# Performance work log

Hardware: AMD Instinct MI355X
Metric: run time of the kernel (lower is better)

The kernel has to match this reference:

```python
import jax, jax.numpy as jnp
import numpy as np

B, L_R, H = 8, 128, 512
CTX_LEN, STATE_NUM, ACT_NUM = 256, 32, 32
L_SRC = CTX_LEN + STATE_NUM + ACT_NUM
N_VOCAB = 32000
N_TOPIC = 4096


def setup_inputs() -> dict:
    key = jax.random.key(0)
    ks = jax.random.split(key, 9)
    return {
        "dec_out": jax.random.normal(ks[0], (B, L_R, H), jnp.float32),
        "src_hidden": jax.random.normal(ks[1], (B, L_SRC, H), jnp.float32),
        "W_gen": jax.random.normal(ks[2], (H, N_VOCAB), jnp.float32) * 0.02,
        "b_gen": jnp.zeros((N_VOCAB,), jnp.float32),
        "src_mask": jax.random.randint(ks[3], (B, 1, L_SRC), 0, 2, jnp.int32),
        "context": jax.random.randint(ks[4], (B, CTX_LEN), 0, N_VOCAB, jnp.int32),
        "tp": jax.random.randint(ks[5], (B, STATE_NUM), 0, N_TOPIC, jnp.int32),
        "action": jax.random.randint(ks[6], (B, ACT_NUM), 0, N_TOPIC, jnp.int32),
        "loc2glo": jax.random.randint(ks[7], (N_TOPIC,), 0, N_VOCAB, jnp.int32),
    }


def _scatter_vocab(prob, idx):
    # prob: [L_r, L_seg], idx: [L_seg] global-vocab ids -> [L_r, n_vocab]
    # duplicate indices accumulate, matching torch scatter_add / one-hot bmm
    return jnp.zeros((prob.shape[0], N_VOCAB), prob.dtype).at[:, idx].add(prob)


def reference(dec_out, src_hidden, W_gen, b_gen, src_mask, context, tp, action, loc2glo):
    # gen logits: [B, L_r, n_vocab]
    gen_logit = jnp.einsum("blh,hv->blv", dec_out, W_gen) + b_gen
    # copy logits over concatenated source: [B, L_r, L_src]
    copy_logit = jnp.einsum("blh,bsh->bls", dec_out, src_hidden)
    copy_logit = jnp.where(src_mask == 0, jnp.float32(-1e9), copy_logit)
    logits = jnp.concatenate([gen_logit, copy_logit], axis=-1)
    logits = logits * (H ** -0.5)  # op.scale_prj
    probs = jax.nn.softmax(logits, axis=-1)

    gen_prob = probs[:, :, :N_VOCAB]
    copy_ctx = probs[:, :, N_VOCAB:N_VOCAB + CTX_LEN]
    copy_tp = probs[:, :, N_VOCAB + CTX_LEN:N_VOCAB + CTX_LEN + STATE_NUM]
    copy_ar = probs[:, :, N_VOCAB + CTX_LEN + STATE_NUM:]

    scatter = jax.vmap(_scatter_vocab)
    ctx_prob = scatter(copy_ctx, context)                 # replaces one-hot bmm
    tp_prob = scatter(copy_tp, loc2glo[tp])               # scatter_add via loc2glo gather
    ar_prob = scatter(copy_ar, loc2glo[action])

    return gen_prob + ctx_prob + tp_prob + ar_prob
```

## Files before the change

kernel.cpp:

```cpp
#include <hip/hip_runtime.h>
#include <stdint.h>
#include <stddef.h>

#define NV    32000
#define HDIM  512
#define LSRC  320
#define MROWS 1024
#define SCALEF 0.044194173824159216f

typedef unsigned short u16;
typedef unsigned int   u32;
typedef __attribute__((ext_vector_type(8))) short short8;
typedef __attribute__((ext_vector_type(4))) float floatx4;

__device__ __forceinline__ u16 f2bf(float f) {
  u32 x = __float_as_uint(f);
  return (u16)((x + 0x7fffu + ((x >> 16) & 1u)) >> 16);
}

typedef __attribute__((address_space(1))) void gvoid;
typedef __attribute__((address_space(3))) void lvoid;
__device__ __forceinline__ void cp16(const u16* g, u16* l) {
  __builtin_amdgcn_global_load_lds((gvoid*)g, (lvoid*)l, 16, 0, 0);
}

__global__ __launch_bounds__(256) void k_convA(const float* __restrict__ dec,
                                               u16* __restrict__ Ab,
                                               float* __restrict__ rowSum) {
  if (blockIdx.x == 0) {
    ((float4*)rowSum)[threadIdx.x] = (float4){0.f, 0.f, 0.f, 0.f};
  }
  int t = blockIdx.x * 256 + threadIdx.x;
  int o = t * 8;
  int tile = o >> 12;
  int mt = tile >> 4, kt = tile & 15;
  int mi = (o & 4095) >> 5, ki = o & 31;
  const float* s = dec + (size_t)(mt * 128 + mi) * HDIM + kt * 32 + ki;
  float4 a = ((const float4*)s)[0];
  float4 b = ((const float4*)s)[1];
  union { u16 h[8]; uint4 v; } pk;
  pk.h[0] = f2bf(a.x); pk.h[1] = f2bf(a.y); pk.h[2] = f2bf(a.z); pk.h[3] = f2bf(a.w);
  pk.h[4] = f2bf(b.x); pk.h[5] = f2bf(b.y); pk.h[6] = f2bf(b.z); pk.h[7] = f2bf(b.w);
  *(uint4*)(Ab + o) = pk.v;
}

__global__ __launch_bounds__(256) void k_convW(const float* __restrict__ W,
                                               u16* __restrict__ Wb) {
  __shared__ u16 lds[128 * 36];
  int tileId = blockIdx.x;
  int nt = tileId >> 4, kt = tileId & 15;
  int t = threadIdx.x;
  const float* src = W + (size_t)kt * 32 * NV + (size_t)nt * 128;
#pragma unroll
  for (int i = 0; i < 4; ++i) {
    int f = t + 256 * i;
    int kin = f >> 5, n4 = f & 31;
    float4 v = *(const float4*)(src + (size_t)kin * NV + n4 * 4);
    int base = (n4 * 4) * 36 + kin;
    lds[base]       = f2bf(v.x);
    lds[base + 36]  = f2bf(v.y);
    lds[base + 72]  = f2bf(v.z);
    lds[base + 108] = f2bf(v.w);
  }
  __syncthreads();
  u16* dst = Wb + (size_t)tileId * 4096;
#pragma unroll
  for (int j = 0; j < 2; ++j) {
    int o = t * 8 + j * 2048;
    int ni = o >> 5, ki0 = o & 31;
    const u16* p = &lds[ni * 36 + ki0];
    uint2 x = *(const uint2*)p;
    uint2 y = *(const uint2*)(p + 4);
    uint4 v; v.x = x.x; v.y = x.y; v.z = y.x; v.w = y.y;
    *(uint4*)(dst + o) = v;
  }
}

__global__ __launch_bounds__(256) void k_convS(const float* __restrict__ srch,
                                               u16* __restrict__ Sb) {
  int t = blockIdx.x * 256 + threadIdx.x;
  int o = t * 8;
  int ki = o & 31;
  int ni = (o >> 5) & 127;
  int kt = (o >> 12) & 15;
  int r  = o >> 16;
  int tile = r % 3, b = r / 3;
  int s = tile * 128 + ni;
  uint4 v;
  if (s < LSRC) {
    const float* p = srch + ((size_t)b * LSRC + s) * HDIM + kt * 32 + ki;
    float4 a = ((const float4*)p)[0];
    float4 c = ((const float4*)p)[1];
    union { u16 h[8]; uint4 u; } pk;
    pk.h[0] = f2bf(a.x); pk.h[1] = f2bf(a.y); pk.h[2] = f2bf(a.z); pk.h[3] = f2bf(a.w);
    pk.h[4] = f2bf(c.x); pk.h[5] = f2bf(c.y); pk.h[6] = f2bf(c.z); pk.h[7] = f2bf(c.w);
    v = pk.u;
  } else {
    v = (uint4){0u, 0u, 0u, 0u};
  }
  *(uint4*)(Sb + o) = v;
}

__global__ __launch_bounds__(256) void k_gemm(const u16* __restrict__ Ab,
                                              const u16* __restrict__ Wb,
                                              const u16* __restrict__ Sb,
                                              const float* __restrict__ bgen,
                                              const int* __restrict__ mask,
                                              u16* __restrict__ wsE,
                                              float* __restrict__ wsCopy,
                                              float* __restrict__ rowSum) {
  __shared__ u16 As[3][4096];
  __shared__ u16 Bs[3][4096];
  int bid = blockIdx.x;
  int x = (bid >> 3) & 7;
  int y = ((bid >> 6) << 3) | (bid & 7);
  if (y >= 253) return;
  int t = threadIdx.x;
  int wid = t >> 6, lane = t & 63;
  int wm = wid >> 1, wn = wid & 1;
  int quad = lane >> 4, l16 = lane & 15;

  const u16* At = Ab + (size_t)x * (16 * 4096);
  const u16* Bt = (y < 250) ? (Wb + (size_t)y * (16 * 4096))
                            : (Sb + (size_t)(x * 3 + (y - 250)) * (16 * 4096));
  const u16* Ag0 = At + wid * 1024 + lane * 8;
  const u16* Bg0 = Bt + wid * 1024 + lane * 8;

  floatx4 acc[4][4];
#pragma unroll
  for (int i = 0; i < 4; ++i)
#pragma unroll
    for (int j = 0; j < 4; ++j) acc[i][j] = (floatx4){0.f, 0.f, 0.f, 0.f};

#pragma unroll
  for (int p = 0; p < 2; ++p) {
    const u16* ag = Ag0 + p * 4096;
    const u16* bg = Bg0 + p * 4096;
    cp16(ag,       &As[p][wid * 1024]);
    cp16(ag + 512, &As[p][wid * 1024 + 512]);
    cp16(bg,       &Bs[p][wid * 1024]);
    cp16(bg + 512, &Bs[p][wid * 1024 + 512]);
  }

#pragma unroll
  for (int kt = 0; kt < 16; ++kt) {
    const int cb = kt % 3;
    asm volatile("s_waitcnt lgkmcnt(0)" ::: "memory");
    if (kt < 15) asm volatile("s_waitcnt vmcnt(4)" ::: "memory");
    else         asm volatile("s_waitcnt vmcnt(0)" ::: "memory");
    __builtin_amdgcn_s_barrier();
    asm volatile("" ::: "memory");
    if (kt < 14) {
      const int sb = (kt + 2) % 3;
      const u16* ag = Ag0 + (kt + 2) * 4096;
      const u16* bg = Bg0 + (kt + 2) * 4096;
      cp16(ag,       &As[sb][wid * 1024]);
      cp16(ag + 512, &As[sb][wid * 1024 + 512]);
      cp16(bg,       &Bs[sb][wid * 1024]);
      cp16(bg + 512, &Bs[sb][wid * 1024 + 512]);
    }
    short8 aR[4], bR[4];
#pragma unroll
    for (int mt = 0; mt < 4; ++mt)
      aR[mt] = *(const short8*)&As[cb][(wm * 64 + mt * 16 + l16) * 32 + quad * 8];
#pragma unroll
    for (int nt = 0; nt < 4; ++nt)
      bR[nt] = *(const short8*)&Bs[cb][(wn * 64 + nt * 16 + l16) * 32 + quad * 8];
#pragma unroll
    for (int mt = 0; mt < 4; ++mt)
#pragma unroll
      for (int nt = 0; nt < 4; ++nt)
        acc[mt][nt] = __builtin_amdgcn_mfma_f32_16x16x32_bf16(aR[mt], bR[nt],
                                                              acc[mt][nt], 0, 0, 0);
  }

  int row0 = x * 128 + wm * 64;
  if (y < 250) {
    int col0 = y * 128 + wn * 64;
    float bg[4];
#pragma unroll
    for (int nt = 0; nt < 4; ++nt) bg[nt] = bgen[col0 + nt * 16 + l16];
#pragma unroll
    for (int mt = 0; mt < 4; ++mt) {
      float rs[4] = {0.f, 0.f, 0.f, 0.f};
#pragma unroll
      for (int nt = 0; nt < 4; ++nt) {
        int col = col0 + nt * 16 + l16;
#pragma unroll
        for (int r = 0; r < 4; ++r) {
          int row = row0 + mt * 16 + quad * 4 + r;
          float e = __expf((acc[mt][nt][r] + bg[nt]) * SCALEF);
          wsE[(size_t)row * NV + col] = f2bf(e);
          rs[r] += e;
        }
      }
#pragma unroll
      for (int r = 0; r < 4; ++r) {
        float v = rs[r];
        v += __shfl_xor(v, 1, 64);
        v += __shfl_xor(v, 2, 64);
        v += __shfl_xor(v, 4, 64);
        v += __shfl_xor(v, 8, 64);
        if (l16 == 0) atomicAdd(&rowSum[row0 + mt * 16 + quad * 4 + r], v);
      }
    }
  } else {
    int b = x;
    int sBase = (y - 250) * 128 + wn * 64;
#pragma unroll
    for (int mt = 0; mt < 4; ++mt) {
      float rs[4] = {0.f, 0.f, 0.f, 0.f};
#pragma unroll
      for (int nt = 0; nt < 4; ++nt) {
        int s = sBase + nt * 16 + l16;
        int valid = (s < LSRC);
        int m = valid ? mask[b * LSRC + s] : 0;
#pragma unroll
        for (int r = 0; r < 4; ++r) {
          int row = row0 + mt * 16 + quad * 4 + r;
          float e = m ? __expf(acc[mt][nt][r] * SCALEF) : 0.f;
          if (valid) wsCopy[row * LSRC + s] = e;
          rs[r] += e;
        }
      }
#pragma unroll
      for (int r = 0; r < 4; ++r) {
        float v = rs[r];
        v += __shfl_xor(v, 1, 64);
        v += __shfl_xor(v, 2, 64);
        v += __shfl_xor(v, 4, 64);
        v += __shfl_xor(v, 8, 64);
        if (l16 == 0) atomicAdd(&rowSum[row0 + mt * 16 + quad * 4 + r], v);
      }
    }
  }
}

__global__ __launch_bounds__(256) void k_norm(const u16* __restrict__ wsE,
                                              const float* __restrict__ wsCopy,
                                              const float* __restrict__ rowSum,
                                              const int* __restrict__ context,
                                              const int* __restrict__ tp,
                                              const int* __restrict__ action,
                                              const int* __restrict__ loc2glo,
                                              float* __restrict__ out) {
  int r = blockIdx.x, b = r >> 7;
  float inv = 1.0f / rowSum[r];
  const uint2* src = (const uint2*)(wsE + (size_t)r * NV);
  float4* dst = (float4*)(out + (size_t)r * NV);
  for (int c = threadIdx.x; c < NV / 4; c += 256) {
    uint2 v = src[c];
    float4 o;
    o.x = __uint_as_float(v.x << 16) * inv;
    o.y = __uint_as_float(v.x & 0xffff0000u) * inv;
    o.z = __uint_as_float(v.y << 16) * inv;
    o.w = __uint_as_float(v.y & 0xffff0000u) * inv;
    dst[c] = o;
  }
  __syncthreads();
  int t = threadIdx.x;
  float* op = out + (size_t)r * NV;
  atomicAdd(op + context[b * 256 + t], wsCopy[r * LSRC + t] * inv);
  if (t < 32) {
    atomicAdd(op + loc2glo[tp[b * 32 + t]],     wsCopy[r * LSRC + 256 + t] * inv);
    atomicAdd(op + loc2glo[action[b * 32 + t]], wsCopy[r * LSRC + 288 + t] * inv);
  }
}

extern "C" void kernel_launch(void* const* d_in, const int* in_sizes, int n_in,
                              void* d_out, int out_size, void* d_ws, size_t ws_size,
                              hipStream_t stream) {
  const float* dec  = (const float*)d_in[0];
  const float* srch = (const float*)d_in[1];
  const float* Wg   = (const float*)d_in[2];
  const float* bg   = (const float*)d_in[3];
  const int*   mask = (const int*)d_in[4];
  const int*   ctx  = (const int*)d_in[5];
  const int*   tp   = (const int*)d_in[6];
  const int*   act  = (const int*)d_in[7];
  const int*   l2g  = (const int*)d_in[8];
  float* out = (float*)d_out;

  char* ws = (char*)d_ws;
  u16*   Wb      = (u16*)(ws);
  u16*   wsE     = (u16*)(ws + 32768000);
  u16*   Ab      = (u16*)(ws + 98304000);
  float* wsCopy  = (float*)(ws + 99352576);
  float* rowSum  = (float*)(ws + 100663296);
  u16*   Sb      = (u16*)(ws + 100667392);

  hipLaunchKernelGGL(k_convA, dim3(256), dim3(256), 0, stream, dec, Ab, rowSum);
  hipLaunchKernelGGL(k_convW, dim3(4000), dim3(256), 0, stream, Wg, Wb);
  hipLaunchKernelGGL(k_convS, dim3(768), dim3(256), 0, stream, srch, Sb);
  hipLaunchKernelGGL(k_gemm, dim3(2048), dim3(256), 0, stream, Ab, Wb, Sb, bg, mask,
                     wsE, wsCopy, rowSum);
  hipLaunchKernelGGL(k_norm, dim3(MROWS), dim3(256), 0, stream, wsE, wsCopy, rowSum,
                     ctx, tp, act, l2g, out);
}
```

Baseline: 346.4 us.

## Merge conversion kernels, transpose MFMA epilogue for vector stores, widen norm blocks

Merges the dec_out and src_hidden bf16 conversion kernels into one launch to save a kernel launch. In the GEMM, the MFMA operands are swapped so each lane holds four consecutive columns of one row. This lets the epilogue write packed 8-byte bf16 and float4 copy values, load bias and mask as vectors, fold the bias and scale into one FMA, and cut the row-sum reduction to two shuffles. s_setprio is placed around the MFMA block, dead copy tiles past LSRC are skipped, and the normalisation kernel moves to 512 threads so the copy scatters run in parallel.

```diff
diff --git a/kernel.cpp b/kernel.cpp
--- a/kernel.cpp
+++ b/kernel.cpp
@@ -24,24 +24,50 @@
   __builtin_amdgcn_global_load_lds((gvoid*)g, (lvoid*)l, 16, 0, 0);
 }
 
-__global__ __launch_bounds__(256) void k_convA(const float* __restrict__ dec,
-                                               u16* __restrict__ Ab,
-                                               float* __restrict__ rowSum) {
-  if (blockIdx.x == 0) {
-    ((float4*)rowSum)[threadIdx.x] = (float4){0.f, 0.f, 0.f, 0.f};
-  }
-  int t = blockIdx.x * 256 + threadIdx.x;
-  int o = t * 8;
-  int tile = o >> 12;
-  int mt = tile >> 4, kt = tile & 15;
-  int mi = (o & 4095) >> 5, ki = o & 31;
-  const float* s = dec + (size_t)(mt * 128 + mi) * HDIM + kt * 32 + ki;
-  float4 a = ((const float4*)s)[0];
-  float4 b = ((const float4*)s)[1];
-  union { u16 h[8]; uint4 v; } pk;
-  pk.h[0] = f2bf(a.x); pk.h[1] = f2bf(a.y); pk.h[2] = f2bf(a.z); pk.h[3] = f2bf(a.w);
-  pk.h[4] = f2bf(b.x); pk.h[5] = f2bf(b.y); pk.h[6] = f2bf(b.z); pk.h[7] = f2bf(b.w);
-  *(uint4*)(Ab + o) = pk.v;
+__global__ __launch_bounds__(256) void k_conv(const float* __restrict__ dec,
+                                              const float* __restrict__ srch,
+                                              u16* __restrict__ Ab,
+                                              u16* __restrict__ Sb,
+                                              float* __restrict__ rowSum) {
+  if (blockIdx.x < 256) {
+    if (blockIdx.x == 0) {
+      ((float4*)rowSum)[threadIdx.x] = (float4){0.f, 0.f, 0.f, 0.f};
+    }
+    int t = blockIdx.x * 256 + threadIdx.x;
+    int o = t * 8;
+    int tile = o >> 12;
+    int mt = tile >> 4, kt = tile & 15;
+    int mi = (o & 4095) >> 5, ki = o & 31;
+    const float* s = dec + (size_t)(mt * 128 + mi) * HDIM + kt * 32 + ki;
+    float4 a = ((const float4*)s)[0];
+    float4 b = ((const float4*)s)[1];
+    union { u16 h[8]; uint4 v; } pk;
+    pk.h[0] = f2bf(a.x); pk.h[1] = f2bf(a.y); pk.h[2] = f2bf(a.z); pk.h[3] = f2bf(a.w);
+    pk.h[4] = f2bf(b.x); pk.h[5] = f2bf(b.y); pk.h[6] = f2bf(b.z); pk.h[7] = f2bf(b.w);
+    *(uint4*)(Ab + o) = pk.v;
+  } else {
+    int t = (blockIdx.x - 256) * 256 + threadIdx.x;
+    int o = t * 8;
+    int ki = o & 31;
+    int ni = (o >> 5) & 127;
+    int kt = (o >> 12) & 15;
+    int r  = o >> 16;
+    int tile = r % 3, b = r / 3;
+    int s = tile * 128 + ni;
+    uint4 v;
+    if (s < LSRC) {
+      const float* p = srch + ((size_t)b * LSRC + s) * HDIM + kt * 32 + ki;
+      float4 a = ((const float4*)p)[0];
+      float4 c = ((const float4*)p)[1];
+      union { u16 h[8]; uint4 u; } pk;
+      pk.h[0] = f2bf(a.x); pk.h[1] = f2bf(a.y); pk.h[2] = f2bf(a.z); pk.h[3] = f2bf(a.w);
+      pk.h[4] = f2bf(c.x); pk.h[5] = f2bf(c.y); pk.h[6] = f2bf(c.z); pk.h[7] = f2bf(c.w);
+      v = pk.u;
+    } else {
+      v = (uint4){0u, 0u, 0u, 0u};
+    }
+    *(uint4*)(Sb + o) = v;
+  }
 }
 
 __global__ __launch_bounds__(256) void k_convW(const float* __restrict__ W,
@@ -74,31 +100,6 @@
     uint4 v; v.x = x.x; v.y = x.y; v.z = y.x; v.w = y.y;
     *(uint4*)(dst + o) = v;
   }
-}
-
-__global__ __launch_bounds__(256) void k_convS(const float* __restrict__ srch,
-                                               u16* __restrict__ Sb) {
-  int t = blockIdx.x * 256 + threadIdx.x;
-  int o = t * 8;
-  int ki = o & 31;
-  int ni = (o >> 5) & 127;
-  int kt = (o >> 12) & 15;
-  int r  = o >> 16;
-  int tile = r % 3, b = r / 3;
-  int s = tile * 128 + ni;
-  uint4 v;
-  if (s < LSRC) {
-    const float* p = srch + ((size_t)b * LSRC + s) * HDIM + kt * 32 + ki;
-    float4 a = ((const float4*)p)[0];
-    float4 c = ((const float4*)p)[1];
-    union { u16 h[8]; uint4 u; } pk;
-    pk.h[0] = f2bf(a.x); pk.h[1] = f2bf(a.y); pk.h[2] = f2bf(a.z); pk.h[3] = f2bf(a.w);
-    pk.h[4] = f2bf(c.x); pk.h[5] = f2bf(c.y); pk.h[6] = f2bf(c.z); pk.h[7] = f2bf(c.w);
-    v = pk.u;
-  } else {
-    v = (uint4){0u, 0u, 0u, 0u};
-  }
-  *(uint4*)(Sb + o) = v;
 }
 
 __global__ __launch_bounds__(256) void k_gemm(const u16* __restrict__ Ab,
@@ -166,77 +167,79 @@
 #pragma unroll
     for (int nt = 0; nt < 4; ++nt)
       bR[nt] = *(const short8*)&Bs[cb][(wn * 64 + nt * 16 + l16) * 32 + quad * 8];
+    __builtin_amdgcn_s_setprio(1);
 #pragma unroll
     for (int mt = 0; mt < 4; ++mt)
 #pragma unroll
       for (int nt = 0; nt < 4; ++nt)
-        acc[mt][nt] = __builtin_amdgcn_mfma_f32_16x16x32_bf16(aR[mt], bR[nt],
+        acc[mt][nt] = __builtin_amdgcn_mfma_f32_16x16x32_bf16(bR[nt], aR[mt],
                                                               acc[mt][nt], 0, 0, 0);
+    __builtin_amdgcn_s_setprio(0);
   }
 
   int row0 = x * 128 + wm * 64;
   if (y < 250) {
     int col0 = y * 128 + wn * 64;
-    float bg[4];
-#pragma unroll
-    for (int nt = 0; nt < 4; ++nt) bg[nt] = bgen[col0 + nt * 16 + l16];
+    float bq[4][4];
+#pragma unroll
+    for (int nt = 0; nt < 4; ++nt) {
+      float4 v = *(const float4*)(bgen + col0 + nt * 16 + quad * 4);
+      bq[nt][0] = v.x * SCALEF; bq[nt][1] = v.y * SCALEF;
+      bq[nt][2] = v.z * SCALEF; bq[nt][3] = v.w * SCALEF;
+    }
 #pragma unroll
     for (int mt = 0; mt < 4; ++mt) {
-      float rs[4] = {0.f, 0.f, 0.f, 0.f};
+      int row = row0 + mt * 16 + l16;
+      float rsum = 0.f;
 #pragma unroll
       for (int nt = 0; nt < 4; ++nt) {
-        int col = col0 + nt * 16 + l16;
-#pragma unroll
-        for (int r = 0; r < 4; ++r) {
-          int row = row0 + mt * 16 + quad * 4 + r;
-          float e = __expf((acc[mt][nt][r] + bg[nt]) * SCALEF);
-          wsE[(size_t)row * NV + col] = f2bf(e);
-          rs[r] += e;
-        }
+        float e0 = __expf(fmaf(acc[mt][nt][0], SCALEF, bq[nt][0]));
+        float e1 = __expf(fmaf(acc[mt][nt][1], SCALEF, bq[nt][1]));
+        float e2 = __expf(fmaf(acc[mt][nt][2], SCALEF, bq[nt][2]));
+        float e3 = __expf(fmaf(acc[mt][nt][3], SCALEF, bq[nt][3]));
+        uint2 pk;
+        pk.x = (u32)f2bf(e0) | ((u32)f2bf(e1) << 16);
+        pk.y = (u32)f2bf(e2) | ((u32)f2bf(e3) << 16);
+        *(uint2*)(wsE + (size_t)row * NV + col0 + nt * 16 + quad * 4) = pk;
+        rsum += (e0 + e1) + (e2 + e3);
       }
-#pragma unroll
-      for (int r = 0; r < 4; ++r) {
-        float v = rs[r];
-        v += __shfl_xor(v, 1, 64);
-        v += __shfl_xor(v, 2, 64);
-        v += __shfl_xor(v, 4, 64);
-        v += __shfl_xor(v, 8, 64);
-        if (l16 == 0) atomicAdd(&rowSum[row0 + mt * 16 + quad * 4 + r], v);
-      }
+      rsum += __shfl_xor(rsum, 16, 64);
+      rsum += __shfl_xor(rsum, 32, 64);
+      if (lane < 16) atomicAdd(&rowSum[row], rsum);
     }
   } else {
     int b = x;
     int sBase = (y - 250) * 128 + wn * 64;
-#pragma unroll
-    for (int mt = 0; mt < 4; ++mt) {
-      float rs[4] = {0.f, 0.f, 0.f, 0.f};
+    if (sBase < LSRC) {
+      int mq[4][4];
 #pragma unroll
       for (int nt = 0; nt < 4; ++nt) {
-        int s = sBase + nt * 16 + l16;
-        int valid = (s < LSRC);
-        int m = valid ? mask[b * LSRC + s] : 0;
-#pragma unroll
-        for (int r = 0; r < 4; ++r) {
-          int row = row0 + mt * 16 + quad * 4 + r;
-          float e = m ? __expf(acc[mt][nt][r] * SCALEF) : 0.f;
-          if (valid) wsCopy[row * LSRC + s] = e;
-          rs[r] += e;
+        int4 v = *(const int4*)(mask + b * LSRC + sBase + nt * 16 + quad * 4);
+        mq[nt][0] = v.x; mq[nt][1] = v.y; mq[nt][2] = v.z; mq[nt][3] = v.w;
+      }
+#pragma unroll
+      for (int mt = 0; mt < 4; ++mt) {
+        int row = row0 + mt * 16 + l16;
+        float rsum = 0.f;
+#pragma unroll
+        for (int nt = 0; nt < 4; ++nt) {
+          float4 ev;
+          ev.x = mq[nt][0] ? __expf(acc[mt][nt][0] * SCALEF) : 0.f;
+          ev.y = mq[nt][1] ? __expf(acc[mt][nt][1] * SCALEF) : 0.f;
+          ev.z = mq[nt][2] ? __expf(acc[mt][nt][2] * SCALEF) : 0.f;
+          ev.w = mq[nt][3] ? __expf(acc[mt][nt][3] * SCALEF) : 0.f;
+          *(float4*)(wsCopy + (size_t)row * LSRC + sBase + nt * 16 + quad * 4) = ev;
+          rsum += (ev.x + ev.y) + (ev.z + ev.w);
         }
+        rsum += __shfl_xor(rsum, 16, 64);
+        rsum += __shfl_xor(rsum, 32, 64);
+        if (lane < 16) atomicAdd(&rowSum[row], rsum);
       }
-#pragma unroll
-      for (int r = 0; r < 4; ++r) {
-        float v = rs[r];
-        v += __shfl_xor(v, 1, 64);
-        v += __shfl_xor(v, 2, 64);
-        v += __shfl_xor(v, 4, 64);
-        v += __shfl_xor(v, 8, 64);
-        if (l16 == 0) atomicAdd(&rowSum[row0 + mt * 16 + quad * 4 + r], v);
-      }
-    }
-  }
-}
-
-__global__ __launch_bounds__(256) void k_norm(const u16* __restrict__ wsE,
+    }
+  }
+}
+
+__global__ __launch_bounds__(512) void k_norm(const u16* __restrict__ wsE,
                                               const float* __restrict__ wsCopy,
                                               const float* __restrict__ rowSum,
                                               const int* __restrict__ context,
@@ -248,7 +251,7 @@
   float inv = 1.0f / rowSum[r];
   const uint2* src = (const uint2*)(wsE + (size_t)r * NV);
   float4* dst = (float4*)(out + (size_t)r * NV);
-  for (int c = threadIdx.x; c < NV / 4; c += 256) {
+  for (int c = threadIdx.x; c < NV / 4; c += 512) {
     uint2 v = src[c];
     float4 o;
     o.x = __uint_as_float(v.x << 16) * inv;
@@ -260,10 +263,14 @@
   __syncthreads();
   int t = threadIdx.x;
   float* op = out + (size_t)r * NV;
-  atomicAdd(op + context[b * 256 + t], wsCopy[r * LSRC + t] * inv);
-  if (t < 32) {
-    atomicAdd(op + loc2glo[tp[b * 32 + t]],     wsCopy[r * LSRC + 256 + t] * inv);
-    atomicAdd(op + loc2glo[action[b * 32 + t]], wsCopy[r * LSRC + 288 + t] * inv);
+  if (t < 256) {
+    atomicAdd(op + context[b * 256 + t], wsCopy[r * LSRC + t] * inv);
+  } else if (t < 288) {
+    int i = t - 256;
+    atomicAdd(op + loc2glo[tp[b * 32 + i]], wsCopy[r * LSRC + 256 + i] * inv);
+  } else if (t < 320) {
+    int i = t - 288;
+    atomicAdd(op + loc2glo[action[b * 32 + i]], wsCopy[r * LSRC + 288 + i] * inv);
   }
 }
 
@@ -289,11 +296,10 @@
   float* rowSum  = (float*)(ws + 100663296);
   u16*   Sb      = (u16*)(ws + 100667392);
 
-  hipLaunchKernelGGL(k_convA, dim3(256), dim3(256), 0, stream, dec, Ab, rowSum);
+  hipLaunchKernelGGL(k_conv, dim3(1024), dim3(256), 0, stream, dec, srch, Ab, Sb, rowSum);
   hipLaunchKernelGGL(k_convW, dim3(4000), dim3(256), 0, stream, Wg, Wb);
-  hipLaunchKernelGGL(k_convS, dim3(768), dim3(256), 0, stream, srch, Sb);
   hipLaunchKernelGGL(k_gemm, dim3(2048), dim3(256), 0, stream, Ab, Wb, Sb, bg, mask,
                      wsE, wsCopy, rowSum);
-  hipLaunchKernelGGL(k_norm, dim3(MROWS), dim3(256), 0, stream, wsE, wsCopy, rowSum,
+  hipLaunchKernelGGL(k_norm, dim3(MROWS), dim3(512), 0, stream, wsE, wsCopy, rowSum,
                      ctx, tp, act, l2g, out);
 }
```

Result: faster. 314.9 us (-9.1%).
